# Kernel optimization log

Hardware: AMD Instinct MI355X
Metric: run time of the kernel (lower is better)

## Reference

```python
import jax, jax.numpy as jnp
import numpy as np
from jax import lax

NUM_GROUP = 512   # G: number of FPS centers
GROUP_SIZE = 32   # S: kNN neighbors per center
BIG = 1e10        # init distance for FPS


def setup_inputs() -> dict:
    key = jax.random.key(0)
    pc = jax.random.normal(key, (16, 8192, 6), dtype=jnp.float32)  # B N C (xyz+normals)
    return {"pc": pc}


def farthest_point_sample(pos, K):
    # pos: [B, N, 3] -> idx: [B, K] (deterministic start at point 0;
    # original uses random_start_point=True, fixed here for reproducibility)
    B, N, _ = pos.shape
    start = jnp.zeros((B,), dtype=jnp.int32)
    dists0 = jnp.full((B, N), BIG, dtype=pos.dtype)

    def step(carry, _):
        dists, last = carry
        lp = jnp.take_along_axis(pos, last[:, None, None], axis=1)  # [B,1,3]
        d = jnp.sum((pos - lp) ** 2, axis=-1)                       # [B,N]
        dists = jnp.minimum(dists, d)
        nxt = jnp.argmax(dists, axis=1).astype(jnp.int32)
        return (dists, nxt), last

    _, idxs = lax.scan(step, (dists0, start), None, length=K)
    return idxs.T  # [B, K]


def knn_indices(q, t, k):
    # q: [B,G,3] queries, t: [B,N,3] targets -> [B,G,k] indices of k nearest
    # squared euclidean gives identical ordering to torch.cdist + topk(smallest)
    d2 = (jnp.sum(q * q, -1)[:, :, None]
          - 2.0 * jnp.einsum('bgd,bnd->bgn', q, t)
          + jnp.sum(t * t, -1)[:, None, :])          # [B,G,N]
    _, idx = lax.top_k(-d2, k)                        # smallest distances
    return idx


def reference(pc):
    B, N, C = pc.shape
    pos = pc[:, :, 0:3]
    rep_idx = farthest_point_sample(pos, NUM_GROUP)                 # [B,G]
    center = jnp.take_along_axis(pc, rep_idx[:, :, None], axis=1)  # [B,G,C]
    nn_idx = knn_indices(center[:, :, 0:3], pos, GROUP_SIZE)        # [B,G,S]
    # knn_gather: [B,G,S,C]
    neighborhood = jax.vmap(lambda p, i: p[i])(pc, nn_idx)
    rel = neighborhood[..., 0:3] - center[:, :, None, 0:3]
    neighborhood = jnp.concatenate([rel, neighborhood[..., 3:]], axis=-1)
    return neighborhood, center, nn_idx
```

## Files before the change

### kernel.cpp

```cpp
#include <hip/hip_runtime.h>

#define NPTS   8192
#define NBATCH 16
#define NGROUP 512
#define GSIZE  32
#define BIGF   1e10f

typedef unsigned long long u64;

template <int CTRL>
__device__ __forceinline__ u64 dpp_max_u64(u64 k) {
    const unsigned lo  = (unsigned)k;
    const unsigned hi  = (unsigned)(k >> 32);
    const unsigned slo = (unsigned)__builtin_amdgcn_update_dpp(0, (int)lo, CTRL, 0xF, 0xF, true);
    const unsigned shi = (unsigned)__builtin_amdgcn_update_dpp(0, (int)hi, CTRL, 0xF, 0xF, true);
    const u64 s = ((u64)shi << 32) | slo;
    return s > k ? s : k;
}

__device__ __forceinline__ u64 umax64(u64 a, u64 b) { return a > b ? a : b; }

__device__ __forceinline__ u64 rdlane64(u64 v, int l) {
    const unsigned lo = (unsigned)__builtin_amdgcn_readlane((int)(unsigned)v, l);
    const unsigned hi = (unsigned)__builtin_amdgcn_readlane((int)(unsigned)(v >> 32), l);
    return ((u64)hi << 32) | lo;
}

__global__ __launch_bounds__(512) void fps_kernel(const float* __restrict__ pc,
                                                  int* __restrict__ rep,
                                                  float4* __restrict__ ws4) {
    const int b    = blockIdx.x;
    const int t    = threadIdx.x;
    const int lane = t & 63;
    const int w    = t >> 6;

    __shared__ float4 sp[NPTS];
    __shared__ __align__(16) u64 keys[2][8];
    __shared__ int lrep[NGROUP];

    const float* base = pc + (size_t)b * NPTS * 6;
    float4* w4 = ws4 + ((size_t)b << 13);

    float px[16], py[16], pz[16], dmin[16];
#pragma unroll
    for (int j = 0; j < 16; ++j) {
        const int p = t * 16 + j;
        const float x = base[p * 6 + 0];
        const float y = base[p * 6 + 1];
        const float z = base[p * 6 + 2];
        px[j] = x; py[j] = y; pz[j] = z;
        const float4 f = make_float4(x, y, z, 0.0f);
        sp[p] = f;
        w4[p] = f;
        dmin[j] = BIGF;
    }
    __syncthreads();

    int last = 0;
    for (int k = 0; k < NGROUP; ++k) {
        if (t == 0) lrep[k] = last;
        if (k == NGROUP - 1) break;

        const float4 L = sp[last];

        float bv = -1.0f;
        int   bi = 0;
#pragma unroll
        for (int j = 0; j < 16; ++j) {
            const float dx = __fsub_rn(px[j], L.x);
            const float dy = __fsub_rn(py[j], L.y);
            const float dz = __fsub_rn(pz[j], L.z);
            const float d = __fadd_rn(__fadd_rn(__fmul_rn(dx, dx),
                                                __fmul_rn(dy, dy)),
                                      __fmul_rn(dz, dz));
            const float dm = fminf(dmin[j], d);
            dmin[j] = dm;
            if (dm > bv) { bv = dm; bi = t * 16 + j; }
        }

        u64 key = ((u64)__float_as_uint(bv) << 13) | (unsigned)(8191 - bi);
        key = dpp_max_u64<0x111>(key);
        key = dpp_max_u64<0x112>(key);
        key = dpp_max_u64<0x114>(key);
        key = dpp_max_u64<0x118>(key);
        key = dpp_max_u64<0x142>(key);
        key = dpp_max_u64<0x143>(key);

        const int buf = k & 1;
        if (lane == 63) keys[buf][w] = key;
        __syncthreads();

        const ulonglong2* kp = (const ulonglong2*)keys[buf];
        const ulonglong2 k0 = kp[0], k1 = kp[1], k2 = kp[2], k3 = kp[3];
        const u64 best = umax64(umax64(umax64(k0.x, k0.y), umax64(k1.x, k1.y)),
                                umax64(umax64(k2.x, k2.y), umax64(k3.x, k3.y)));
        last = 8191 - (int)(best & 0x1FFFull);
    }

    __syncthreads();
    for (int j = t; j < NGROUP; j += 512)
        rep[b * NGROUP + j] = lrep[j];
}

__global__ __launch_bounds__(256) void knn_kernel(const float* __restrict__ pc,
                                                  const float4* __restrict__ ws4,
                                                  const int* __restrict__ rep,
                                                  float* __restrict__ out) {
    const int tid  = threadIdx.x;
    const int lane = tid & 63;
    const int w    = tid >> 6;
    const int q    = blockIdx.x * 4 + w;
    const int b    = q >> 9;

    const float*  base  = pc  + (size_t)b * NPTS * 6;
    const float4* base4 = ws4 + ((size_t)b << 13);
    const int     r     = rep[q];

    const float4 Q = base4[r];
    const float qxf = Q.x, qyf = Q.y, qzf = Q.z;
    const double qx = (double)qxf, qy = (double)qyf, qz = (double)qzf;

    const u64 INFB = 0x7ff0000000000000ull;
    u64 vk = INFB;  int vi = 0x7fffffff;
    u64 tauk = INFB;

    for (int i = 0; i < NPTS / 128; ++i) {
        const int p0 = i * 128 + lane;
        const float4 T0 = base4[p0];
        const float4 T1 = base4[p0 + 64];

        const double dx0 = qx - (double)T0.x;
        const double dy0 = qy - (double)T0.y;
        const double dz0 = qz - (double)T0.z;
        const u64 kd0 = __double_as_longlong(dx0 * dx0 + dy0 * dy0 + dz0 * dz0);
        const double dx1 = qx - (double)T1.x;
        const double dy1 = qy - (double)T1.y;
        const double dz1 = qz - (double)T1.z;
        const u64 kd1 = __double_as_longlong(dx1 * dx1 + dy1 * dy1 + dz1 * dz1);

        u64 m0 = __ballot(kd0 < tauk);
        const u64 m1pre = __ballot(kd1 < tauk);

        if (m0 | m1pre) {
            while (m0) {
                const int l = __ffsll(m0) - 1;
                m0 &= m0 - 1;
                const u64 xk = rdlane64(kd0, l);
                const int xi = i * 128 + l;
                const u64 pk = __shfl_up(vk, 1);
                const int pv = __shfl_up(vi, 1);
                const bool ltp = (lane > 0) && (xk < pk);
                const bool ltc = xk < vk;
                vk = ltp ? pk : (ltc ? xk : vk);
                vi = ltp ? pv : (ltc ? xi : vi);
            }
            tauk = rdlane64(vk, 31);
            u64 m1 = m1pre;
            while (m1) {
                const int l = __ffsll(m1) - 1;
                m1 &= m1 - 1;
                const u64 xk = rdlane64(kd1, l);
                if (xk < tauk) {
                    const int xi = i * 128 + 64 + l;
                    const u64 pk = __shfl_up(vk, 1);
                    const int pv = __shfl_up(vi, 1);
                    const bool ltp = (lane > 0) && (xk < pk);
                    const bool ltc = xk < vk;
                    vk = ltp ? pk : (ltc ? xk : vk);
                    vi = ltp ? pv : (ltc ? xi : vi);
                }
            }
            tauk = rdlane64(vk, 31);
        }
    }

    const size_t NBH = (size_t)NBATCH * NGROUP * GSIZE * 6;
    const size_t CEN = (size_t)NBATCH * NGROUP * 6;

    if (lane == 0) {
#pragma unroll
        for (int c = 0; c < 6; ++c)
            out[NBH + (size_t)q * 6 + c] = base[r * 6 + c];
    }
    if (lane < GSIZE) {
        const int n = vi;
        out[NBH + CEN + (size_t)q * GSIZE + lane] = (float)n;

        const float* np_ = base + (size_t)n * 6;
        const size_t o = ((size_t)q * GSIZE + lane) * 6;
        out[o + 0] = __fsub_rn(np_[0], qxf);
        out[o + 1] = __fsub_rn(np_[1], qyf);
        out[o + 2] = __fsub_rn(np_[2], qzf);
        out[o + 3] = np_[3];
        out[o + 4] = np_[4];
        out[o + 5] = np_[5];
    }
}

extern "C" void kernel_launch(void* const* d_in, const int* in_sizes, int n_in,
                              void* d_out, int out_size, void* d_ws, size_t ws_size,
                              hipStream_t stream) {
    const float* pc  = (const float*)d_in[0];
    float*       out = (float*)d_out;
    int*         rep = (int*)d_ws;
    float4*      ws4 = (float4*)((char*)d_ws + 32 * 1024);

    fps_kernel<<<NBATCH, 512, 0, stream>>>(pc, rep, ws4);
    knn_kernel<<<NBATCH * NGROUP / 4, 256, 0, stream>>>(pc, ws4, rep, out);
}
```

Before: 653.7 us.

## Overlap kNN with FPS via a persistent fused kernel and per-center ready flags

Merges FPS and kNN into one launch. Sixteen blocks run FPS and publish each chosen center index to global memory as soon as it is selected. The remaining 240 blocks spin-wait on those flags and run the kNN search for each center while FPS is still in progress. A small prepack kernel writes the float4 xyz copy and resets the flags to -1. The goal is to hide the kNN stage behind the serial FPS loop. The cost is polling overhead and a dependence on all 256 blocks being resident at the same time; if they are not, the spin-wait can deadlock.

```diff
diff --git a/kernel.cpp b/kernel.cpp
--- a/kernel.cpp
+++ b/kernel.cpp
@@ -26,96 +26,19 @@
     return ((u64)hi << 32) | lo;
 }
 
-__global__ __launch_bounds__(512) void fps_kernel(const float* __restrict__ pc,
-                                                  int* __restrict__ rep,
-                                                  float4* __restrict__ ws4) {
-    const int b    = blockIdx.x;
-    const int t    = threadIdx.x;
-    const int lane = t & 63;
-    const int w    = t >> 6;
-
-    __shared__ float4 sp[NPTS];
-    __shared__ __align__(16) u64 keys[2][8];
-    __shared__ int lrep[NGROUP];
-
-    const float* base = pc + (size_t)b * NPTS * 6;
-    float4* w4 = ws4 + ((size_t)b << 13);
-
-    float px[16], py[16], pz[16], dmin[16];
-#pragma unroll
-    for (int j = 0; j < 16; ++j) {
-        const int p = t * 16 + j;
-        const float x = base[p * 6 + 0];
-        const float y = base[p * 6 + 1];
-        const float z = base[p * 6 + 2];
-        px[j] = x; py[j] = y; pz[j] = z;
-        const float4 f = make_float4(x, y, z, 0.0f);
-        sp[p] = f;
-        w4[p] = f;
-        dmin[j] = BIGF;
-    }
-    __syncthreads();
-
-    int last = 0;
-    for (int k = 0; k < NGROUP; ++k) {
-        if (t == 0) lrep[k] = last;
-        if (k == NGROUP - 1) break;
-
-        const float4 L = sp[last];
-
-        float bv = -1.0f;
-        int   bi = 0;
-#pragma unroll
-        for (int j = 0; j < 16; ++j) {
-            const float dx = __fsub_rn(px[j], L.x);
-            const float dy = __fsub_rn(py[j], L.y);
-            const float dz = __fsub_rn(pz[j], L.z);
-            const float d = __fadd_rn(__fadd_rn(__fmul_rn(dx, dx),
-                                                __fmul_rn(dy, dy)),
-                                      __fmul_rn(dz, dz));
-            const float dm = fminf(dmin[j], d);
-            dmin[j] = dm;
-            if (dm > bv) { bv = dm; bi = t * 16 + j; }
-        }
-
-        u64 key = ((u64)__float_as_uint(bv) << 13) | (unsigned)(8191 - bi);
-        key = dpp_max_u64<0x111>(key);
-        key = dpp_max_u64<0x112>(key);
-        key = dpp_max_u64<0x114>(key);
-        key = dpp_max_u64<0x118>(key);
-        key = dpp_max_u64<0x142>(key);
-        key = dpp_max_u64<0x143>(key);
-
-        const int buf = k & 1;
-        if (lane == 63) keys[buf][w] = key;
-        __syncthreads();
-
-        const ulonglong2* kp = (const ulonglong2*)keys[buf];
-        const ulonglong2 k0 = kp[0], k1 = kp[1], k2 = kp[2], k3 = kp[3];
-        const u64 best = umax64(umax64(umax64(k0.x, k0.y), umax64(k1.x, k1.y)),
-                                umax64(umax64(k2.x, k2.y), umax64(k3.x, k3.y)));
-        last = 8191 - (int)(best & 0x1FFFull);
-    }
-
-    __syncthreads();
-    for (int j = t; j < NGROUP; j += 512)
-        rep[b * NGROUP + j] = lrep[j];
-}
-
-__global__ __launch_bounds__(256) void knn_kernel(const float* __restrict__ pc,
-                                                  const float4* __restrict__ ws4,
-                                                  const int* __restrict__ rep,
-                                                  float* __restrict__ out) {
-    const int tid  = threadIdx.x;
-    const int lane = tid & 63;
-    const int w    = tid >> 6;
-    const int q    = blockIdx.x * 4 + w;
-    const int b    = q >> 9;
-
-    const float*  base  = pc  + (size_t)b * NPTS * 6;
-    const float4* base4 = ws4 + ((size_t)b << 13);
-    const int     r     = rep[q];
-
+__global__ __launch_bounds__(256) void prepack_kernel(const float* __restrict__ pc,
+                                                      float4* __restrict__ ws4,
+                                                      int* __restrict__ rep) {
+    const int i = blockIdx.x * 256 + threadIdx.x;
+    const float* s = pc + (size_t)i * 6;
+    ws4[i] = make_float4(s[0], s[1], s[2], 0.0f);
+    if (i < NBATCH * NGROUP) rep[i] = -1;
+}
+
+__device__ __forceinline__ void knn_one(const float* __restrict__ base,
+                                        const float4* __restrict__ base4,
+                                        float* __restrict__ out,
+                                        const int q, const int r, const int lane) {
     const float4 Q = base4[r];
     const float qxf = Q.x, qyf = Q.y, qzf = Q.z;
     const double qx = (double)qxf, qy = (double)qyf, qz = (double)qzf;
@@ -197,6 +120,100 @@
     }
 }
 
+__global__ __launch_bounds__(512) void fused_kernel(const float* __restrict__ pc,
+                                                    const float4* __restrict__ ws4,
+                                                    int* __restrict__ rep,
+                                                    float* __restrict__ out) {
+    const int bid  = blockIdx.x;
+    const int t    = threadIdx.x;
+    const int lane = t & 63;
+    const int w    = t >> 6;
+
+    __shared__ float4 sp[NPTS];
+    __shared__ __align__(16) u64 keys[2][8];
+
+    if (bid < NBATCH) {
+        const int b = bid;
+        const float* base = pc + (size_t)b * NPTS * 6;
+
+        float px[16], py[16], pz[16], dmin[16];
+#pragma unroll
+        for (int j = 0; j < 16; ++j) {
+            const int p = t * 16 + j;
+            const float x = base[p * 6 + 0];
+            const float y = base[p * 6 + 1];
+            const float z = base[p * 6 + 2];
+            px[j] = x; py[j] = y; pz[j] = z;
+            sp[p] = make_float4(x, y, z, 0.0f);
+            dmin[j] = BIGF;
+        }
+        __syncthreads();
+
+        int last = 0;
+        for (int k = 0; k < NGROUP; ++k) {
+            if (t == 0)
+                __hip_atomic_store(rep + b * NGROUP + k, last,
+                                   __ATOMIC_RELAXED, __HIP_MEMORY_SCOPE_AGENT);
+            if (k == NGROUP - 1) break;
+
+            const float4 L = sp[last];
+
+            float bv = -1.0f;
+            int   bi = 0;
+#pragma unroll
+            for (int j = 0; j < 16; ++j) {
+                const float dx = __fsub_rn(px[j], L.x);
+                const float dy = __fsub_rn(py[j], L.y);
+                const float dz = __fsub_rn(pz[j], L.z);
+                const float d = __fadd_rn(__fadd_rn(__fmul_rn(dx, dx),
+                                                    __fmul_rn(dy, dy)),
+                                          __fmul_rn(dz, dz));
+                const float dm = fminf(dmin[j], d);
+                dmin[j] = dm;
+                if (dm > bv) { bv = dm; bi = t * 16 + j; }
+            }
+
+            u64 key = ((u64)__float_as_uint(bv) << 13) | (unsigned)(8191 - bi);
+            key = dpp_max_u64<0x111>(key);
+            key = dpp_max_u64<0x112>(key);
+            key = dpp_max_u64<0x114>(key);
+            key = dpp_max_u64<0x118>(key);
+            key = dpp_max_u64<0x142>(key);
+            key = dpp_max_u64<0x143>(key);
+
+            const int buf = k & 1;
+            if (lane == 63) keys[buf][w] = key;
+            __syncthreads();
+
+            const ulonglong2* kp = (const ulonglong2*)keys[buf];
+            const ulonglong2 k0 = kp[0], k1 = kp[1], k2 = kp[2], k3 = kp[3];
+            const u64 best = umax64(umax64(umax64(k0.x, k0.y), umax64(k1.x, k1.y)),
+                                    umax64(umax64(k2.x, k2.y), umax64(k3.x, k3.y)));
+            last = 8191 - (int)(best & 0x1FFFull);
+        }
+    } else {
+        const int kb = bid - NBATCH;
+        const int b  = kb / 15;
+        const int j  = kb % 15;
+        const int m0 = j * 8 + w;
+
+        const float*  base  = pc  + (size_t)b * NPTS * 6;
+        const float4* base4 = ws4 + ((size_t)b << 13);
+
+        for (int m = m0; m < NGROUP; m += 120) {
+            const int q = b * NGROUP + m;
+            int rv;
+            for (;;) {
+                rv = __hip_atomic_load(rep + q, __ATOMIC_RELAXED,
+                                       __HIP_MEMORY_SCOPE_AGENT);
+                if (rv >= 0) break;
+                __builtin_amdgcn_s_sleep(8);
+            }
+            knn_one(base, base4, out, q, rv, lane);
+        }
+    }
+}
+
 extern "C" void kernel_launch(void* const* d_in, const int* in_sizes, int n_in,
                               void* d_out, int out_size, void* d_ws, size_t ws_size,
                               hipStream_t stream) {
@@ -205,6 +222,6 @@
     int*         rep = (int*)d_ws;
     float4*      ws4 = (float4*)((char*)d_ws + 32 * 1024);
 
-    fps_kernel<<<NBATCH, 512, 0, stream>>>(pc, rep, ws4);
-    knn_kernel<<<NBATCH * NGROUP / 4, 256, 0, stream>>>(pc, ws4, rep, out);
-}
+    prepack_kernel<<<NBATCH * NPTS / 256, 256, 0, stream>>>(pc, ws4, rep);
+    fused_kernel<<<NBATCH + 240, 512, 0, stream>>>(pc, ws4, rep, out);
+}
```

Measured after the change: 586.3 us. 1.11x faster.
